# Kernel optimization log

Measured on AMD Instinct MI355X. Metric: run time of the kernel, lower is better.

The kernel has to match this reference:

```python
import jax, jax.numpy as jnp
import numpy as np

N_QUBITS = 22
DIM = 2 ** N_QUBITS


def setup_inputs() -> dict:
    key = jax.random.key(0)
    k1, k2, k3, k4 = jax.random.split(key, 4)
    state = jax.random.normal(k1, (DIM,), dtype=jnp.float32)
    state = state / jnp.linalg.norm(state)
    rabi = jax.random.uniform(k2, (N_QUBITS,), dtype=jnp.float32)
    detune = jax.random.uniform(k3, (N_QUBITS,), dtype=jnp.float32)
    # U = triu(normal^2, k=1) flattened upper triangle -> interaction strengths
    U_params = jax.random.normal(k4, (N_QUBITS * (N_QUBITS - 1) // 2,), dtype=jnp.float32) ** 2
    return {"state": state, "rabi": rabi, "detune": detune, "U_params": U_params}


def reference(state, rabi, detune, U_params):
    # H|psi> = sum_i (rabi_i/2) X_i |psi> + sum_i (-detune_i) N_i |psi>
    #        + sum_{i<j} U_ij N_i N_j |psi>
    n = rabi.shape[0]
    dim = state.shape[0]
    # bit value of qubit i for each basis index k (qubit 0 = most significant,
    # matching state.reshape((2,)*n) axis ordering)
    idx = jnp.arange(dim, dtype=jnp.uint32)
    shifts = jnp.arange(n - 1, -1, -1, dtype=jnp.uint32)
    bits = ((idx[:, None] >> shifts[None, :]) & 1).astype(state.dtype)  # [dim, n]
    iu, ju = np.triu_indices(n, k=1)
    Umat = jnp.zeros((n, n), dtype=state.dtype).at[iu, ju].set(U_params)
    # diagonal part: detuning (Number ops) + pairwise interactions (N_i N_j)
    diag = bits @ (-detune) + jnp.sum((bits @ Umat) * bits, axis=1)  # [dim]
    out = diag * state
    # off-diagonal Rabi part: X_i flips qubit i
    st = state.reshape((2,) * n)
    for i in range(n):
        out = out + (0.5 * rabi[i]) * jnp.flip(st, axis=i).reshape(-1)
    return out
```

## Files before the change

### kernel.cpp

```cpp
#include <hip/hip_runtime.h>


#define THREADS 512
#define NBLK 512

typedef float fvec4 __attribute__((ext_vector_type(4)));

__device__ __forceinline__ int uidx(int i, int j) {
    return i * (43 - i) / 2 + (j - i - 1);
}

__global__ __launch_bounds__(THREADS, 4) void ryd_kernel(
        const float* __restrict__ state, const float* __restrict__ rabi,
        const float* __restrict__ detune, const float* __restrict__ U,
        float* __restrict__ out) {
    __shared__ float4 tileS[2048];
    __shared__ __align__(16) float dloS[2048];
    __shared__ float Us[231];
    __shared__ float dets[22];
    __shared__ float CJ[4][11];
    __shared__ float S4v[4];

    const float4* __restrict__ sF4 = (const float4*)state;
    float4* __restrict__ oF4 = (float4*)out;
    const unsigned t = threadIdx.x;
    const unsigned blk = blockIdx.x;
    const unsigned tile = ((blk & 7u) << 6) | (blk >> 3);
    const unsigned tbase = tile * 2048u;

    if (t < 231u) Us[t] = U[t];
    else if (t < 253u) dets[t - 231u] = detune[t - 231u];

    float4 vreg[4];
#pragma unroll
    for (int c = 0; c < 4; ++c)
        vreg[c] = sF4[tbase + t + 512u * (unsigned)c];
    float4 pgl[2][3];
#pragma unroll
    for (int b = 6; b < 9; ++b)
        pgl[0][b - 6] = sF4[(tbase + t) ^ (2048u << b)];

    __syncthreads();

    {
        float base = 0.f, R9 = 0.f, R10 = 0.f;
#pragma unroll
        for (int j2 = 0; j2 < 9; ++j2) {
            if ((t >> j2) & 1u) {
                base -= dets[21 - j2];
#pragma unroll
                for (int j1 = 0; j1 < j2; ++j1)
                    if ((t >> j1) & 1u) base += Us[uidx(21 - j2, 21 - j1)];
                R9  += Us[uidx(12, 21 - j2)];
                R10 += Us[uidx(11, 21 - j2)];
            }
        }
        const float w9  = -dets[12];
        const float w10 = -dets[11];
        const float u910 = Us[uidx(11, 12)];
        dloS[t]         = base;
        dloS[t + 512u]  = base + w9 + R9;
        dloS[t + 1024u] = base + w10 + R10;
        dloS[t + 1536u] = base + w9 + R9 + w10 + R10 + u910;
    }
    if (t < 44u) {
        const int c = (int)t / 11, j = (int)t % 11;
        const unsigned h = (tile << 2) | (unsigned)c;
        float cc = 0.f;
        for (int jh = 0; jh < 11; ++jh)
            if ((h >> jh) & 1u) cc += Us[uidx(10 - jh, 21 - j)];
        CJ[c][j] = cc;
    } else if (t < 48u) {
        const int c = (int)t - 44;
        const unsigned h = (tile << 2) | (unsigned)c;
        float s = 0.f;
        for (int j2 = 0; j2 < 11; ++j2) {
            if ((h >> j2) & 1u) {
                s -= dets[10 - j2];
                for (int j1 = 0; j1 < j2; ++j1)
                    if ((h >> j1) & 1u) s += Us[uidx(10 - j2, 10 - j1)];
            }
        }
        S4v[c] = s;
    }

#pragma unroll
    for (int c = 0; c < 4; ++c)
        tileS[t + 512u * (unsigned)c] = vreg[c];
    __syncthreads();

    const float r0 = 0.5f * rabi[21];
    const float r1 = 0.5f * rabi[20];
    float cb[9];
#pragma unroll
    for (int b = 0; b < 9; ++b) cb[b] = 0.5f * rabi[8 - b];

#pragma unroll
    for (int c = 0; c < 4; ++c) {
        const unsigned f = t + 512u * (unsigned)c;
        const unsigned F = tbase + f;
        float4 pg[6];
#pragma unroll
        for (int b = 0; b < 6; ++b)
            pg[b] = sF4[F ^ (2048u << b)];
        if (c < 3) {
#pragma unroll
            for (int b = 6; b < 9; ++b)
                pgl[(c + 1) & 1][b - 6] = sF4[(F + 512u) ^ (2048u << b)];
        }

        float cj[11];
#pragma unroll
        for (int j = 0; j < 11; ++j) cj[j] = CJ[c][j];
        float s = S4v[c];
        const unsigned m = f & 511u;
#pragma unroll
        for (int j = 0; j < 9; ++j)
            s += ((m >> j) & 1u) ? cj[j + 2] : 0.f;
        const float4 dl = ((const float4*)dloS)[m];
        const float4 v = vreg[c];
        const float d0 = s + dl.x;
        const float d1 = s + cj[0] + dl.y;
        const float d2 = s + cj[1] + dl.z;
        const float d3 = s + cj[0] + cj[1] + dl.w;
        float4 acc;
        acc.x = d0 * v.x; acc.y = d1 * v.y; acc.z = d2 * v.z; acc.w = d3 * v.w;
        acc.x += r0 * v.y; acc.y += r0 * v.x; acc.z += r0 * v.w; acc.w += r0 * v.z;
        acc.x += r1 * v.z; acc.y += r1 * v.w; acc.z += r1 * v.x; acc.w += r1 * v.y;
#pragma unroll
        for (int b = 2; b <= 12; ++b) {
            const float rb = 0.5f * rabi[21 - b];
            const float4 p = tileS[f ^ (1u << (b - 2))];
            acc.x += rb * p.x; acc.y += rb * p.y; acc.z += rb * p.z; acc.w += rb * p.w;
        }
#pragma unroll
        for (int b = 0; b < 6; ++b) {
            acc.x += cb[b] * pg[b].x; acc.y += cb[b] * pg[b].y;
            acc.z += cb[b] * pg[b].z; acc.w += cb[b] * pg[b].w;
        }
#pragma unroll
        for (int q = 0; q < 3; ++q) {
            const float4 p = pgl[c & 1][q];
            acc.x += cb[6 + q] * p.x; acc.y += cb[6 + q] * p.y;
            acc.z += cb[6 + q] * p.z; acc.w += cb[6 + q] * p.w;
        }
        union { float4 s4; fvec4 v4; } u;
        u.s4 = acc;
        __builtin_nontemporal_store(u.v4, reinterpret_cast<fvec4*>(oF4 + F));
    }
}

extern "C" void kernel_launch(void* const* d_in, const int* in_sizes, int n_in,
                              void* d_out, int out_size, void* d_ws, size_t ws_size,
                              hipStream_t stream) {
    const float* state  = (const float*)d_in[0];
    const float* rabi   = (const float*)d_in[1];
    const float* detune = (const float*)d_in[2];
    const float* U      = (const float*)d_in[3];
    float* out = (float*)d_out;
    (void)in_sizes; (void)n_in; (void)out_size; (void)d_ws; (void)ws_size;

    hipLaunchKernelGGL(ryd_kernel, dim3(NBLK), dim3(THREADS), 0, stream,
                       state, rabi, detune, U, out);
}
```

Before: 21.09 us.

## Halve tile size, compute diagonal in registers, and hoist uniform coefficients to SGPRs

Each block now handles 1024 float4 entries instead of 2048, with twice as many blocks. The low-bit diagonal table in shared memory is replaced by per-thread register values. One extra qubit moves from shared-memory exchange to an in-register swap between the two vregs, and one more moves to global gather. Uniform Rabi and CJ coefficients are forced into scalar registers with readfirstlane. The aim is less LDS traffic and better occupancy, but each block reads more global memory for partner elements (7+3 strided reads per element).

```diff
diff --git a/kernel.cpp b/kernel.cpp
--- a/kernel.cpp
+++ b/kernel.cpp
@@ -2,7 +2,7 @@
 
 
 #define THREADS 512
-#define NBLK 512
+#define NBLK 1024
 
 typedef float fvec4 __attribute__((ext_vector_type(4)));
 
@@ -10,69 +10,70 @@
     return i * (43 - i) / 2 + (j - i - 1);
 }
 
+__device__ __forceinline__ float to_sgpr(float x) {
+    return __uint_as_float(__builtin_amdgcn_readfirstlane(__float_as_uint(x)));
+}
+
 __global__ __launch_bounds__(THREADS, 4) void ryd_kernel(
         const float* __restrict__ state, const float* __restrict__ rabi,
         const float* __restrict__ detune, const float* __restrict__ U,
         float* __restrict__ out) {
-    __shared__ float4 tileS[2048];
-    __shared__ __align__(16) float dloS[2048];
+    __shared__ float4 tileS[1024];
     __shared__ float Us[231];
     __shared__ float dets[22];
-    __shared__ float CJ[4][11];
-    __shared__ float S4v[4];
+    __shared__ float CJ[2][11];
+    __shared__ float S2v[2];
 
     const float4* __restrict__ sF4 = (const float4*)state;
     float4* __restrict__ oF4 = (float4*)out;
     const unsigned t = threadIdx.x;
     const unsigned blk = blockIdx.x;
-    const unsigned tile = ((blk & 7u) << 6) | (blk >> 3);
-    const unsigned tbase = tile * 2048u;
+    const unsigned hf = ((blk & 7u) << 7) | (blk >> 3);
+    const unsigned tbase = hf * 1024u;
 
     if (t < 231u) Us[t] = U[t];
     else if (t < 253u) dets[t - 231u] = detune[t - 231u];
 
-    float4 vreg[4];
-#pragma unroll
-    for (int c = 0; c < 4; ++c)
-        vreg[c] = sF4[tbase + t + 512u * (unsigned)c];
+    float4 vreg[2];
+    vreg[0] = sF4[tbase + t];
+    vreg[1] = sF4[tbase + t + 512u];
     float4 pgl[2][3];
 #pragma unroll
-    for (int b = 6; b < 9; ++b)
-        pgl[0][b - 6] = sF4[(tbase + t) ^ (2048u << b)];
+    for (int j = 0; j < 3; ++j)
+        pgl[0][j] = sF4[(tbase + t) ^ (1024u << (7 + j))];
 
     __syncthreads();
 
+    float dlx, dly, dlz, dlw;
     {
-        float base = 0.f, R9 = 0.f, R10 = 0.f;
+        float B = 0.f, R0 = 0.f, R1 = 0.f;
 #pragma unroll
         for (int j2 = 0; j2 < 9; ++j2) {
-            if ((t >> j2) & 1u) {
-                base -= dets[21 - j2];
+            const int q2 = 19 - j2;
+            float ap = -dets[q2];
 #pragma unroll
-                for (int j1 = 0; j1 < j2; ++j1)
-                    if ((t >> j1) & 1u) base += Us[uidx(21 - j2, 21 - j1)];
-                R9  += Us[uidx(12, 21 - j2)];
-                R10 += Us[uidx(11, 21 - j2)];
-            }
+            for (int j1 = 0; j1 < j2; ++j1)
+                ap += ((t >> j1) & 1u) ? Us[uidx(q2, 19 - j1)] : 0.f;
+            const bool b2 = (t >> j2) & 1u;
+            B  += b2 ? ap : 0.f;
+            R0 += b2 ? Us[uidx(q2, 21)] : 0.f;
+            R1 += b2 ? Us[uidx(q2, 20)] : 0.f;
         }
-        const float w9  = -dets[12];
-        const float w10 = -dets[11];
-        const float u910 = Us[uidx(11, 12)];
-        dloS[t]         = base;
-        dloS[t + 512u]  = base + w9 + R9;
-        dloS[t + 1024u] = base + w10 + R10;
-        dloS[t + 1536u] = base + w9 + R9 + w10 + R10 + u910;
+        const float w0 = -dets[21] + R0;
+        const float w1 = -dets[20] + R1;
+        dlx = B; dly = B + w0; dlz = B + w1;
+        dlw = B + w0 + w1 + Us[uidx(20, 21)];
     }
-    if (t < 44u) {
+    if (t < 22u) {
         const int c = (int)t / 11, j = (int)t % 11;
-        const unsigned h = (tile << 2) | (unsigned)c;
+        const unsigned h = (hf << 1) | (unsigned)c;
         float cc = 0.f;
         for (int jh = 0; jh < 11; ++jh)
             if ((h >> jh) & 1u) cc += Us[uidx(10 - jh, 21 - j)];
         CJ[c][j] = cc;
-    } else if (t < 48u) {
-        const int c = (int)t - 44;
-        const unsigned h = (tile << 2) | (unsigned)c;
+    } else if (t < 24u) {
+        const int c = (int)t - 22;
+        const unsigned h = (hf << 1) | (unsigned)c;
         float s = 0.f;
         for (int j2 = 0; j2 < 11; ++j2) {
             if ((h >> j2) & 1u) {
@@ -81,68 +82,75 @@
                     if ((h >> j1) & 1u) s += Us[uidx(10 - j2, 10 - j1)];
             }
         }
-        S4v[c] = s;
+        S2v[c] = s;
     }
 
-#pragma unroll
-    for (int c = 0; c < 4; ++c)
-        tileS[t + 512u * (unsigned)c] = vreg[c];
+    tileS[t] = vreg[0];
+    tileS[t + 512u] = vreg[1];
     __syncthreads();
 
-    const float r0 = 0.5f * rabi[21];
-    const float r1 = 0.5f * rabi[20];
-    float cb[9];
+    const float r0   = to_sgpr(0.5f * rabi[21]);
+    const float r1   = to_sgpr(0.5f * rabi[20]);
+    const float rb11 = to_sgpr(0.5f * rabi[10]);
+    float rls[9];
 #pragma unroll
-    for (int b = 0; b < 9; ++b) cb[b] = 0.5f * rabi[8 - b];
+    for (int j = 0; j < 9; ++j) rls[j] = to_sgpr(0.5f * rabi[19 - j]);
+    float cbs[10];
+#pragma unroll
+    for (int j = 0; j < 10; ++j) cbs[j] = to_sgpr(0.5f * rabi[9 - j]);
 
 #pragma unroll
-    for (int c = 0; c < 4; ++c) {
+    for (int c = 0; c < 2; ++c) {
         const unsigned f = t + 512u * (unsigned)c;
         const unsigned F = tbase + f;
-        float4 pg[6];
+        float4 pg[7];
 #pragma unroll
-        for (int b = 0; b < 6; ++b)
-            pg[b] = sF4[F ^ (2048u << b)];
-        if (c < 3) {
+        for (int j = 0; j < 7; ++j)
+            pg[j] = sF4[F ^ (1024u << j)];
+        if (c == 0) {
 #pragma unroll
-            for (int b = 6; b < 9; ++b)
-                pgl[(c + 1) & 1][b - 6] = sF4[(F + 512u) ^ (2048u << b)];
+            for (int j = 0; j < 3; ++j)
+                pgl[1][j] = sF4[(F + 512u) ^ (1024u << (7 + j))];
         }
 
         float cj[11];
 #pragma unroll
-        for (int j = 0; j < 11; ++j) cj[j] = CJ[c][j];
-        float s = S4v[c];
-        const unsigned m = f & 511u;
+        for (int j = 0; j < 11; ++j) cj[j] = to_sgpr(CJ[c][j]);
+        float s = to_sgpr(S2v[c]);
 #pragma unroll
         for (int j = 0; j < 9; ++j)
-            s += ((m >> j) & 1u) ? cj[j + 2] : 0.f;
-        const float4 dl = ((const float4*)dloS)[m];
+            s += ((t >> j) & 1u) ? cj[j + 2] : 0.f;
         const float4 v = vreg[c];
-        const float d0 = s + dl.x;
-        const float d1 = s + cj[0] + dl.y;
-        const float d2 = s + cj[1] + dl.z;
-        const float d3 = s + cj[0] + cj[1] + dl.w;
+        const float d0 = s + dlx;
+        const float d1 = s + cj[0] + dly;
+        const float d2 = s + cj[1] + dlz;
+        const float d3 = s + cj[0] + cj[1] + dlw;
         float4 acc;
         acc.x = d0 * v.x; acc.y = d1 * v.y; acc.z = d2 * v.z; acc.w = d3 * v.w;
         acc.x += r0 * v.y; acc.y += r0 * v.x; acc.z += r0 * v.w; acc.w += r0 * v.z;
         acc.x += r1 * v.z; acc.y += r1 * v.w; acc.z += r1 * v.x; acc.w += r1 * v.y;
-#pragma unroll
-        for (int b = 2; b <= 12; ++b) {
-            const float rb = 0.5f * rabi[21 - b];
-            const float4 p = tileS[f ^ (1u << (b - 2))];
-            acc.x += rb * p.x; acc.y += rb * p.y; acc.z += rb * p.z; acc.w += rb * p.w;
+        {
+            const float4 p = vreg[c ^ 1];
+            acc.x += rb11 * p.x; acc.y += rb11 * p.y;
+            acc.z += rb11 * p.z; acc.w += rb11 * p.w;
         }
 #pragma unroll
-        for (int b = 0; b < 6; ++b) {
-            acc.x += cb[b] * pg[b].x; acc.y += cb[b] * pg[b].y;
-            acc.z += cb[b] * pg[b].z; acc.w += cb[b] * pg[b].w;
+        for (int j = 0; j < 9; ++j) {
+            const float4 p = tileS[f ^ (1u << j)];
+            acc.x += rls[j] * p.x; acc.y += rls[j] * p.y;
+            acc.z += rls[j] * p.z; acc.w += rls[j] * p.w;
         }
 #pragma unroll
-        for (int q = 0; q < 3; ++q) {
-            const float4 p = pgl[c & 1][q];
-            acc.x += cb[6 + q] * p.x; acc.y += cb[6 + q] * p.y;
-            acc.z += cb[6 + q] * p.z; acc.w += cb[6 + q] * p.w;
+        for (int j = 0; j < 3; ++j) {
+            const float4 p = pgl[c][j];
+            acc.x += cbs[7 + j] * p.x; acc.y += cbs[7 + j] * p.y;
+            acc.z += cbs[7 + j] * p.z; acc.w += cbs[7 + j] * p.w;
+        }
+#pragma unroll
+        for (int j = 0; j < 7; ++j) {
+            const float4 p = pg[j];
+            acc.x += cbs[j] * p.x; acc.y += cbs[j] * p.y;
+            acc.z += cbs[j] * p.z; acc.w += cbs[j] * p.w;
         }
         union { float4 s4; fvec4 v4; } u;
         u.s4 = acc;
```

Measured after the change: 24.64 us. 16.9% more time.
